# Kernel optimization log

Hardware: AMD Instinct MI355X
Metric: run time of the kernel (lower is better)

Reference implementation:

```python
import jax, jax.numpy as jnp
import numpy as np

NUM_HEADS = 8
GEM_P = 3.0
GEM_EPS = 1e-6
L2_EPS = 1e-12


def _l2norm(x):
    n = jnp.sqrt(jnp.sum(x * x, axis=-1, keepdims=True))
    return x / jnp.maximum(n, L2_EPS)


def setup_inputs() -> dict:
    key = jax.random.key(0)
    ks = jax.random.split(key, 7)
    B, Ci, H, W = 8, 256, 40, 40
    D, N = 128, 32768
    image_feat = jax.random.normal(ks[0], (B, Ci, H, W), dtype=jnp.float32)
    cloud_feat = jax.random.normal(ks[1], (N, D), dtype=jnp.float32)
    cloud_bids = jax.random.randint(ks[2], (N,), 0, B, dtype=jnp.int32)
    W1 = jax.random.normal(ks[3], (Ci, D), dtype=jnp.float32) * (1.0 / np.sqrt(Ci))
    b1 = jnp.zeros((D,), dtype=jnp.float32)
    W2 = jax.random.normal(ks[4], (D, Ci), dtype=jnp.float32) * (1.0 / np.sqrt(D))
    b2 = jnp.zeros((Ci,), dtype=jnp.float32)
    return {"image_feat": image_feat, "cloud_feat": cloud_feat, "cloud_bids": cloud_bids,
            "W1": W1, "b1": b1, "W2": W2, "b2": b2}


def _gem(x, axis):
    # generalized-mean pooling: (mean(clamp(x,eps)^p))^(1/p)
    xp = jnp.clip(x, GEM_EPS, None) ** GEM_P
    return jnp.mean(xp, axis=axis) ** (1.0 / GEM_P)


def reference(image_feat, cloud_feat, cloud_bids, W1, b1, W2, b2):
    B, Ci, H, W = image_feat.shape
    D = W1.shape[1]
    h, dh = NUM_HEADS, D // NUM_HEADS

    # image branch: permute -> linear -> tokens
    x = jnp.einsum('bchw,cd->bhwd', image_feat, W1) + b1          # [B,H,W,D]
    tok = _l2norm(x.reshape(B, H * W, D))                          # [B,HW,D]

    # window_size=1 SA: all image tokens of a batch share coord (b,0,0,0)
    # -> full self-attention per batch window; use_proj=False -> q=k=v=feats
    q = tok.reshape(B, H * W, h, dh)
    scores = jnp.einsum('bnhd,bmhd->bhnm', q, q) * (dh ** -0.5)    # [B,h,HW,HW]
    attn = jax.nn.softmax(scores, axis=-1)
    out = jnp.einsum('bhnm,bmhd->bnhd', attn, q).reshape(B, H, W, D)

    # cloud tokens: unique voxel coords -> singleton windows -> identity attention
    cloud_out = _l2norm(cloud_feat)                                # [N,D]

    # project image tokens back to image_dim channels
    img_out = jnp.einsum('bhwd,dc->bhwc', out, W2) + b2            # [B,H,W,Ci]
    img_out = jnp.transpose(img_out, (0, 3, 1, 2))                 # [B,Ci,H,W]

    # GeM pooling
    image_gem = _gem(img_out, axis=(2, 3))                         # [B,Ci]
    cp = jnp.clip(cloud_out, GEM_EPS, None) ** GEM_P
    seg = jax.ops.segment_sum(cp, cloud_bids, num_segments=B)      # [B,D]
    cnt = jax.ops.segment_sum(jnp.ones((cloud_out.shape[0], 1), cp.dtype),
                              cloud_bids, num_segments=B)
    cloud_gem = (seg / jnp.maximum(cnt, 1.0)) ** (1.0 / GEM_P)     # [B,D]

    return (img_out, cloud_out, image_gem, cloud_gem)
```

## Files before the change

### kernel.cpp

```cpp
#include <hip/hip_runtime.h>
#include <hip/hip_bf16.h>
#include <math.h>

#define BATCH 8
#define CI    256
#define HWSZ  1600
#define DDIM  128
#define NHEAD 8
#define DH    16
#define NPTS  32768

typedef __attribute__((ext_vector_type(4))) short s16x4;
typedef __attribute__((ext_vector_type(4))) float f32x4;

#if defined(__HIP_DEVICE_COMPILE__)
  #if __has_builtin(__builtin_amdgcn_mfma_f32_16x16x16bf16_1k)
    #define MFMA16(a, b, c) __builtin_amdgcn_mfma_f32_16x16x16bf16_1k(a, b, c, 0, 0, 0)
  #elif __has_builtin(__builtin_amdgcn_mfma_f32_16x16x16_bf16)
    #define MFMA16(a, b, c) __builtin_amdgcn_mfma_f32_16x16x16_bf16(a, b, c, 0, 0, 0)
  #else
    #error "no 16x16x16 bf16 mfma builtin on this device target"
  #endif
  #if __has_builtin(__builtin_amdgcn_exp2f)
    #define EXP2(x) __builtin_amdgcn_exp2f(x)
  #else
    #define EXP2(x) exp2f(x)
  #endif
#else
  #define MFMA16(a, b, c) (c)
  #define EXP2(x) (x)
#endif

union fragu {
  s16x4 s;
  unsigned int u[2];
  uint2 u2;
};

__device__ __forceinline__ unsigned int pk_bf2(float a, float b) {
  __hip_bfloat162 h = __float22bfloat162_rn(make_float2(a, b));
  return *(unsigned int*)&h;
}
__device__ __forceinline__ float bf2f(unsigned short u) {
  return __uint_as_float(((unsigned int)u) << 16);
}

__global__ __launch_bounds__(256) void kprep(
    const float* __restrict__ W1, const float* __restrict__ W2,
    const float* __restrict__ cf, const int* __restrict__ bids,
    unsigned short* __restrict__ W1s, unsigned short* __restrict__ W2s,
    float* __restrict__ cloud_out, float* __restrict__ gaw,
    float* __restrict__ cntw) {
  __shared__ float ga[BATCH * DDIM];
  __shared__ float gc[BATCH];
  int t = threadIdx.x;
  if (blockIdx.x < 64) {
    int e = blockIdx.x * 256 + t;
    int lane = e & 63, lm = lane & 15, qd = lane >> 4;
    if (e < 8192) {
      int ks = (e >> 6) & 15, dt = e >> 10;
      const float* p = W1 + (size_t)(ks * 16 + 4 * qd) * DDIM + dt * 16 + lm;
      float f0 = p[0], f1 = p[DDIM], f2 = p[2 * DDIM], f3 = p[3 * DDIM];
      *(uint2*)&W1s[(size_t)e * 4] = make_uint2(pk_bf2(f0, f1), pk_bf2(f2, f3));
    } else {
      int e2 = e - 8192;
      int ks = (e2 >> 6) & 7, ct = e2 >> 9;
      const float* p = W2 + (size_t)(ks * 16 + 4 * qd) * CI + ct * 16 + lm;
      float f0 = p[0], f1 = p[CI], f2 = p[2 * CI], f3 = p[3 * CI];
      *(uint2*)&W2s[(size_t)e2 * 4] = make_uint2(pk_bf2(f0, f1), pk_bf2(f2, f3));
    }
    return;
  }
  int bk = blockIdx.x - 64;
  for (int i = t; i < BATCH * DDIM; i += 256) ga[i] = 0.f;
  if (t < BATCH) gc[t] = 0.f;
  __syncthreads();
  for (int half = 0; half < 2; half++) {
    int r = bk * 128 + half * 64 + (t >> 2);
    int dq = (t & 3) * 32;
    const float* row = cf + (size_t)r * DDIM + dq;
    float4 v[8];
    float ss = 0.f;
#pragma unroll
    for (int j = 0; j < 8; j++) {
      v[j] = *(const float4*)(row + j * 4);
      ss += v[j].x*v[j].x + v[j].y*v[j].y + v[j].z*v[j].z + v[j].w*v[j].w;
    }
    ss += __shfl_xor(ss, 1);
    ss += __shfl_xor(ss, 2);
    float sc = 1.f / fmaxf(sqrtf(ss), 1e-12f);
    int bid = bids[r];
    if ((t & 3) == 0) atomicAdd(&gc[bid], 1.f);
    float* orow = cloud_out + (size_t)r * DDIM + dq;
    float* gb = &ga[bid * DDIM + dq];
#pragma unroll
    for (int j = 0; j < 8; j++) {
      float4 y;
      y.x = v[j].x * sc; y.y = v[j].y * sc; y.z = v[j].z * sc; y.w = v[j].w * sc;
      *(float4*)(orow + j * 4) = y;
      float c0 = fmaxf(y.x, 1e-6f), c1 = fmaxf(y.y, 1e-6f);
      float c2 = fmaxf(y.z, 1e-6f), c3 = fmaxf(y.w, 1e-6f);
      atomicAdd(&gb[j*4+0], c0*c0*c0);
      atomicAdd(&gb[j*4+1], c1*c1*c1);
      atomicAdd(&gb[j*4+2], c2*c2*c2);
      atomicAdd(&gb[j*4+3], c3*c3*c3);
    }
  }
  __syncthreads();
  for (int i = t; i < BATCH * DDIM; i += 256) gaw[(size_t)bk * 1024 + i] = ga[i];
  if (t < BATCH) cntw[bk * 8 + t] = gc[t];
}

__global__ __launch_bounds__(256) void k1_mfma(
    const float* __restrict__ img, const unsigned short* __restrict__ W1s,
    const float* __restrict__ b1, unsigned short* __restrict__ tokh) {
  int t = threadIdx.x, lane = t & 63, w = t >> 6;
  int lm = lane & 15, qd = lane >> 4;
  int blk = blockIdx.x;
  int b = blk / 25, n0 = (blk % 25) * 64;
  int tok = n0 + w * 16 + lm;
  const float* imgb = img + (size_t)b * CI * HWSZ;
  const s16x4* W1s4 = (const s16x4*)W1s;
  float fv[16][4];
#pragma unroll
  for (int ks = 0; ks < 16; ks++) {
    const float* p = imgb + (size_t)(ks * 16 + 4 * qd) * HWSZ + tok;
    fv[ks][0] = p[0];        fv[ks][1] = p[HWSZ];
    fv[ks][2] = p[2 * HWSZ]; fv[ks][3] = p[3 * HWSZ];
  }
  f32x4 acc[8];
#pragma unroll
  for (int dt = 0; dt < 8; dt++) acc[dt] = (f32x4){0.f, 0.f, 0.f, 0.f};
#pragma unroll
  for (int ks = 0; ks < 16; ks++) {
    fragu bf_;
    bf_.u[0] = pk_bf2(fv[ks][0], fv[ks][1]);
    bf_.u[1] = pk_bf2(fv[ks][2], fv[ks][3]);
#pragma unroll
    for (int dt = 0; dt < 8; dt++) {
      s16x4 af = W1s4[(dt * 16 + ks) * 64 + lane];
      acc[dt] = MFMA16(af, bf_.s, acc[dt]);
    }
  }
  float vals[8][4];
  float ss = 0.f;
#pragma unroll
  for (int dt = 0; dt < 8; dt++)
#pragma unroll
    for (int r = 0; r < 4; r++) {
      float v = acc[dt][r] + b1[dt * 16 + 4 * qd + r];
      vals[dt][r] = v;
      ss += v * v;
    }
  ss += __shfl_xor(ss, 16);
  ss += __shfl_xor(ss, 32);
  float inv = 1.f / fmaxf(sqrtf(ss), 1e-12f);
#pragma unroll
  for (int dt = 0; dt < 8; dt++) {
    uint2 pk = make_uint2(pk_bf2(vals[dt][0] * inv, vals[dt][1] * inv),
                          pk_bf2(vals[dt][2] * inv, vals[dt][3] * inv));
    *(uint2*)&tokh[(((size_t)b * NHEAD + dt) * HWSZ + tok) * DH + 4 * qd] = pk;
  }
}

#define NKC2     800
#define XK_STR   24
#define VT_STR   808
__global__ __launch_bounds__(512) void k2_attn(
    const unsigned short* __restrict__ tokh, float* __restrict__ numw,
    float* __restrict__ denw) {
  __shared__ unsigned short sXk[NKC2 * XK_STR];
  __shared__ unsigned short sVt[16 * VT_STR];
  const int gx = blockIdx.x;
  const int bh = gx >> 1, kc = gx & 1;
  const int t = threadIdx.x;
  const int lane = t & 63;
  const int w = t >> 6;
  const int lm = lane & 15;
  const int qd = lane >> 4;
  const unsigned short* tok = tokh + (size_t)bh * (HWSZ * DH);
  const int qw = blockIdx.y * 512 + w * 64;
  const bool active = qw < HWSZ;

  for (int r = t; r < NKC2; r += 512) {
    const uint4* src = (const uint4*)(tok + (size_t)(kc * NKC2 + r) * DH);
    union { uint4 u4[2]; unsigned short us[16]; } uu;
    uu.u4[0] = src[0]; uu.u4[1] = src[1];
    *(uint4*)&sXk[r * XK_STR]     = uu.u4[0];
    *(uint4*)&sXk[r * XK_STR + 8] = uu.u4[1];
#pragma unroll
    for (int d = 0; d < 16; d++) sVt[d * VT_STR + r] = uu.us[d];
  }

  const float SCL = 0.25f * 1.44269504088896f;
  s16x4 qf[4];
  f32x4 oacc[4];
  f32x4 dacc[4];
#pragma unroll
  for (int s = 0; s < 4; s++) {
    oacc[s] = (f32x4){0.f, 0.f, 0.f, 0.f};
    dacc[s] = (f32x4){0.f, 0.f, 0.f, 0.f};
  }
  if (active) {
#pragma unroll
    for (int s = 0; s < 4; s++) {
      const unsigned short* qs = tok + (size_t)(qw + s * 16 + lm) * DH + 4 * qd;
      s16x4 raw = *(const s16x4*)qs;
      fragu q;
      q.u[0] = pk_bf2(bf2f((unsigned short)raw[0]) * SCL,
                      bf2f((unsigned short)raw[1]) * SCL);
      q.u[1] = pk_bf2(bf2f((unsigned short)raw[2]) * SCL,
                      bf2f((unsigned short)raw[3]) * SCL);
      qf[s] = q.s;
    }
  }
  __syncthreads();

  if (active) {
    fragu ones;
    ones.u[0] = 0x3F803F80u;
    ones.u[1] = 0x3F803F80u;
#pragma unroll 2
    for (int st = 0; st < NKC2 / 16; st++) {
      int n0 = st * 16;
      s16x4 kf = *(const s16x4*)&sXk[(n0 + lm) * XK_STR + 4 * qd];
      s16x4 vf = *(const s16x4*)&sVt[lm * VT_STR + n0 + 4 * qd];
#pragma unroll
      for (int s = 0; s < 4; s++) {
        f32x4 sc = MFMA16(kf, qf[s], ((f32x4){0.f, 0.f, 0.f, 0.f}));
        float e0 = EXP2(sc.x), e1 = EXP2(sc.y), e2 = EXP2(sc.z), e3 = EXP2(sc.w);
        fragu pf;
        pf.u[0] = pk_bf2(e0, e1);
        pf.u[1] = pk_bf2(e2, e3);
        dacc[s] = MFMA16(ones.s, pf.s, dacc[s]);
        oacc[s] = MFMA16(vf, pf.s, oacc[s]);
      }
    }
  }

  if (active) {
#pragma unroll
    for (int s = 0; s < 4; s++) {
      size_t q = (size_t)qw + s * 16 + lm;
      float* np = numw + (((size_t)bh * 2 + kc) * HWSZ + q) * 16 + 4 * qd;
      *(f32x4*)np = oacc[s];
      if (qd == 0) denw[((size_t)bh * 2 + kc) * HWSZ + q] = dacc[s][0];
    }
  }
}

__global__ __launch_bounds__(256) void k3_mfma(
    const float* __restrict__ numw, const float* __restrict__ denw,
    const unsigned short* __restrict__ W2s, const float* __restrict__ b2,
    float* __restrict__ img_out) {
  int t = threadIdx.x, lane = t & 63, w = t >> 6;
  int lm = lane & 15, qd = lane >> 4;
  int blk = blockIdx.x;
  int b = blk / 25, n0 = (blk % 25) * 64;
  int tok = n0 + w * 16 + lm;
  const s16x4* W2s4 = (const s16x4*)W2s;
  f32x4 acc[16];
#pragma unroll
  for (int ct = 0; ct < 16; ct++) acc[ct] = (f32x4){0.f, 0.f, 0.f, 0.f};
#pragma unroll 2
  for (int ks = 0; ks < 8; ks++) {
    size_t bh2 = (size_t)(b * 8 + ks) * 2;
    const float* npb = numw + (bh2 * HWSZ + tok) * 16 + 4 * qd;
    f32x4 nv0 = *(const f32x4*)npb;
    f32x4 nv1 = *(const f32x4*)(npb + (size_t)HWSZ * 16);
    float d0 = denw[bh2 * HWSZ + tok];
    float d1 = denw[bh2 * HWSZ + HWSZ + tok];
    float inv = 1.f / (d0 + d1);
    fragu bf_;
    bf_.u[0] = pk_bf2((nv0.x + nv1.x) * inv, (nv0.y + nv1.y) * inv);
    bf_.u[1] = pk_bf2((nv0.z + nv1.z) * inv, (nv0.w + nv1.w) * inv);
#pragma unroll
    for (int ct = 0; ct < 16; ct++) {
      s16x4 af = W2s4[(ct * 8 + ks) * 64 + lane];
      acc[ct] = MFMA16(af, bf_.s, acc[ct]);
    }
  }
  float* ob = img_out + (size_t)b * CI * HWSZ;
#pragma unroll
  for (int ct = 0; ct < 16; ct++)
#pragma unroll
    for (int r = 0; r < 4; r++) {
      int ci = ct * 16 + 4 * qd + r;
      ob[(size_t)ci * HWSZ + tok] = acc[ct][r] + b2[ci];
    }
}

__global__ __launch_bounds__(256) void kpost(
    const float* __restrict__ img_out, const float* __restrict__ gaw,
    const float* __restrict__ cntw, float* __restrict__ image_gem,
    float* __restrict__ cloud_gem) {
  __shared__ float cs[BATCH];
  int t = threadIdx.x;
  if (blockIdx.x < 512) {
    int w = t >> 6, lane = t & 63;
    int row = blockIdx.x * 4 + w;
    const float* r = img_out + (size_t)row * HWSZ;
    float s = 0.f;
    for (int i = lane; i < HWSZ; i += 64) {
      float c = fmaxf(r[i], 1e-6f);
      s += c * c * c;
    }
    s += __shfl_xor(s, 1);  s += __shfl_xor(s, 2);  s += __shfl_xor(s, 4);
    s += __shfl_xor(s, 8);  s += __shfl_xor(s, 16); s += __shfl_xor(s, 32);
    if (lane == 0) image_gem[row] = powf(s * (1.f / (float)HWSZ), 1.f / 3.f);
  } else {
    int j = (blockIdx.x - 512) * 256 + t;
    if (t < BATCH) {
      float s = 0.f;
      for (int k = 0; k < 256; k++) s += cntw[k * 8 + t];
      cs[t] = s;
    }
    __syncthreads();
    float s = 0.f;
#pragma unroll 4
    for (int k = 0; k < 256; k++) s += gaw[(size_t)k * 1024 + j];
    int b = j >> 7;
    cloud_gem[j] = powf(s / fmaxf(cs[b], 1.f), 1.f / 3.f);
  }
}

extern "C" void kernel_launch(void* const* d_in, const int* in_sizes, int n_in,
                              void* d_out, int out_size, void* d_ws, size_t ws_size,
                              hipStream_t stream) {
  const float* image_feat = (const float*)d_in[0];
  const float* cloud_feat = (const float*)d_in[1];
  const int*   cloud_bids = (const int*)d_in[2];
  const float* W1 = (const float*)d_in[3];
  const float* b1 = (const float*)d_in[4];
  const float* W2 = (const float*)d_in[5];
  const float* b2 = (const float*)d_in[6];

  float* out = (float*)d_out;
  float* img_out   = out;
  float* cloud_out = out + 3276800;
  float* image_gem = out + 3276800 + 4194304;
  float* cloud_gem = image_gem + 2048;

  char* ws = (char*)d_ws;
  unsigned short* tokh = (unsigned short*)ws;
  float* numw = (float*)(ws + 3276800);
  float* denw = (float*)(ws + 16384000);
  unsigned short* W1s = (unsigned short*)(ws + 17203200);
  unsigned short* W2s = (unsigned short*)(ws + 17268736);
  float* gaw  = (float*)(ws + 17334272);
  float* cntw = (float*)(ws + 18382848);

  kprep<<<dim3(320), dim3(256), 0, stream>>>(W1, W2, cloud_feat, cloud_bids,
                                             W1s, W2s, cloud_out, gaw, cntw);
  k1_mfma<<<dim3(200), dim3(256), 0, stream>>>(image_feat, W1s, b1, tokh);
  k2_attn<<<dim3(128, 4), dim3(512), 0, stream>>>(tokh, numw, denw);
  k3_mfma<<<dim3(200), dim3(256), 0, stream>>>(numw, denw, W2s, b2, img_out);
  kpost<<<dim3(516), dim3(256), 0, stream>>>(img_out, gaw, cntw,
                                             image_gem, cloud_gem);
}
```

Baseline: 192.7 us.

## Fuse image GeM reduction into projection epilogue and move cloud work into k1

The image GeM cube-sum is now computed in the k3 epilogue from register values, using cross-lane shuffles and global atomics into a zeroed buffer. This removes kpost's second pass over the 13 MB img_out tensor. The cloud L2-norm and segment-sum blocks move from kprep into k1 as extra blocks, so they run alongside the image projection, and kprep shrinks to weight packing plus zeroing the accumulator. The cost is float atomics, which make the summation order nondeterministic, plus shuffle overhead in k3.

```diff
diff --git a/kernel.cpp b/kernel.cpp
--- a/kernel.cpp
+++ b/kernel.cpp
@@ -47,74 +47,80 @@
 
 __global__ __launch_bounds__(256) void kprep(
     const float* __restrict__ W1, const float* __restrict__ W2,
+    unsigned short* __restrict__ W1s, unsigned short* __restrict__ W2s,
+    float* __restrict__ gsum) {
+  int t = threadIdx.x;
+  if (blockIdx.x == 64) {
+    for (int i = t; i < BATCH * CI; i += 256) gsum[i] = 0.f;
+    return;
+  }
+  int e = blockIdx.x * 256 + t;
+  int lane = e & 63, lm = lane & 15, qd = lane >> 4;
+  if (e < 8192) {
+    int ks = (e >> 6) & 15, dt = e >> 10;
+    const float* p = W1 + (size_t)(ks * 16 + 4 * qd) * DDIM + dt * 16 + lm;
+    float f0 = p[0], f1 = p[DDIM], f2 = p[2 * DDIM], f3 = p[3 * DDIM];
+    *(uint2*)&W1s[(size_t)e * 4] = make_uint2(pk_bf2(f0, f1), pk_bf2(f2, f3));
+  } else {
+    int e2 = e - 8192;
+    int ks = (e2 >> 6) & 7, ct = e2 >> 9;
+    const float* p = W2 + (size_t)(ks * 16 + 4 * qd) * CI + ct * 16 + lm;
+    float f0 = p[0], f1 = p[CI], f2 = p[2 * CI], f3 = p[3 * CI];
+    *(uint2*)&W2s[(size_t)e2 * 4] = make_uint2(pk_bf2(f0, f1), pk_bf2(f2, f3));
+  }
+}
+
+__global__ __launch_bounds__(256) void k1_mfma(
+    const float* __restrict__ img, const unsigned short* __restrict__ W1s,
+    const float* __restrict__ b1, unsigned short* __restrict__ tokh,
     const float* __restrict__ cf, const int* __restrict__ bids,
-    unsigned short* __restrict__ W1s, unsigned short* __restrict__ W2s,
     float* __restrict__ cloud_out, float* __restrict__ gaw,
     float* __restrict__ cntw) {
   __shared__ float ga[BATCH * DDIM];
   __shared__ float gc[BATCH];
   int t = threadIdx.x;
-  if (blockIdx.x < 64) {
-    int e = blockIdx.x * 256 + t;
-    int lane = e & 63, lm = lane & 15, qd = lane >> 4;
-    if (e < 8192) {
-      int ks = (e >> 6) & 15, dt = e >> 10;
-      const float* p = W1 + (size_t)(ks * 16 + 4 * qd) * DDIM + dt * 16 + lm;
-      float f0 = p[0], f1 = p[DDIM], f2 = p[2 * DDIM], f3 = p[3 * DDIM];
-      *(uint2*)&W1s[(size_t)e * 4] = make_uint2(pk_bf2(f0, f1), pk_bf2(f2, f3));
-    } else {
-      int e2 = e - 8192;
-      int ks = (e2 >> 6) & 7, ct = e2 >> 9;
-      const float* p = W2 + (size_t)(ks * 16 + 4 * qd) * CI + ct * 16 + lm;
-      float f0 = p[0], f1 = p[CI], f2 = p[2 * CI], f3 = p[3 * CI];
-      *(uint2*)&W2s[(size_t)e2 * 4] = make_uint2(pk_bf2(f0, f1), pk_bf2(f2, f3));
-    }
+  if (blockIdx.x >= 200) {
+    int bk = blockIdx.x - 200;
+    for (int i = t; i < BATCH * DDIM; i += 256) ga[i] = 0.f;
+    if (t < BATCH) gc[t] = 0.f;
+    __syncthreads();
+    for (int half = 0; half < 2; half++) {
+      int r = bk * 128 + half * 64 + (t >> 2);
+      int dq = (t & 3) * 32;
+      const float* row = cf + (size_t)r * DDIM + dq;
+      float4 v[8];
+      float ss = 0.f;
+#pragma unroll
+      for (int j = 0; j < 8; j++) {
+        v[j] = *(const float4*)(row + j * 4);
+        ss += v[j].x*v[j].x + v[j].y*v[j].y + v[j].z*v[j].z + v[j].w*v[j].w;
+      }
+      ss += __shfl_xor(ss, 1);
+      ss += __shfl_xor(ss, 2);
+      float sc = 1.f / fmaxf(sqrtf(ss), 1e-12f);
+      int bid = bids[r];
+      if ((t & 3) == 0) atomicAdd(&gc[bid], 1.f);
+      float* orow = cloud_out + (size_t)r * DDIM + dq;
+      float* gb = &ga[bid * DDIM + dq];
+#pragma unroll
+      for (int j = 0; j < 8; j++) {
+        float4 y;
+        y.x = v[j].x * sc; y.y = v[j].y * sc; y.z = v[j].z * sc; y.w = v[j].w * sc;
+        *(float4*)(orow + j * 4) = y;
+        float c0 = fmaxf(y.x, 1e-6f), c1 = fmaxf(y.y, 1e-6f);
+        float c2 = fmaxf(y.z, 1e-6f), c3 = fmaxf(y.w, 1e-6f);
+        atomicAdd(&gb[j*4+0], c0*c0*c0);
+        atomicAdd(&gb[j*4+1], c1*c1*c1);
+        atomicAdd(&gb[j*4+2], c2*c2*c2);
+        atomicAdd(&gb[j*4+3], c3*c3*c3);
+      }
+    }
+    __syncthreads();
+    for (int i = t; i < BATCH * DDIM; i += 256) gaw[(size_t)bk * 1024 + i] = ga[i];
+    if (t < BATCH) cntw[bk * 8 + t] = gc[t];
     return;
   }
-  int bk = blockIdx.x - 64;
-  for (int i = t; i < BATCH * DDIM; i += 256) ga[i] = 0.f;
-  if (t < BATCH) gc[t] = 0.f;
-  __syncthreads();
-  for (int half = 0; half < 2; half++) {
-    int r = bk * 128 + half * 64 + (t >> 2);
-    int dq = (t & 3) * 32;
-    const float* row = cf + (size_t)r * DDIM + dq;
-    float4 v[8];
-    float ss = 0.f;
-#pragma unroll
-    for (int j = 0; j < 8; j++) {
-      v[j] = *(const float4*)(row + j * 4);
-      ss += v[j].x*v[j].x + v[j].y*v[j].y + v[j].z*v[j].z + v[j].w*v[j].w;
-    }
-    ss += __shfl_xor(ss, 1);
-    ss += __shfl_xor(ss, 2);
-    float sc = 1.f / fmaxf(sqrtf(ss), 1e-12f);
-    int bid = bids[r];
-    if ((t & 3) == 0) atomicAdd(&gc[bid], 1.f);
-    float* orow = cloud_out + (size_t)r * DDIM + dq;
-    float* gb = &ga[bid * DDIM + dq];
-#pragma unroll
-    for (int j = 0; j < 8; j++) {
-      float4 y;
-      y.x = v[j].x * sc; y.y = v[j].y * sc; y.z = v[j].z * sc; y.w = v[j].w * sc;
-      *(float4*)(orow + j * 4) = y;
-      float c0 = fmaxf(y.x, 1e-6f), c1 = fmaxf(y.y, 1e-6f);
-      float c2 = fmaxf(y.z, 1e-6f), c3 = fmaxf(y.w, 1e-6f);
-      atomicAdd(&gb[j*4+0], c0*c0*c0);
-      atomicAdd(&gb[j*4+1], c1*c1*c1);
-      atomicAdd(&gb[j*4+2], c2*c2*c2);
-      atomicAdd(&gb[j*4+3], c3*c3*c3);
-    }
-  }
-  __syncthreads();
-  for (int i = t; i < BATCH * DDIM; i += 256) gaw[(size_t)bk * 1024 + i] = ga[i];
-  if (t < BATCH) cntw[bk * 8 + t] = gc[t];
-}
-
-__global__ __launch_bounds__(256) void k1_mfma(
-    const float* __restrict__ img, const unsigned short* __restrict__ W1s,
-    const float* __restrict__ b1, unsigned short* __restrict__ tokh) {
-  int t = threadIdx.x, lane = t & 63, w = t >> 6;
+  int lane = t & 63, w = t >> 6;
   int lm = lane & 15, qd = lane >> 4;
   int blk = blockIdx.x;
   int b = blk / 25, n0 = (blk % 25) * 64;
@@ -252,7 +258,7 @@
 __global__ __launch_bounds__(256) void k3_mfma(
     const float* __restrict__ numw, const float* __restrict__ denw,
     const unsigned short* __restrict__ W2s, const float* __restrict__ b2,
-    float* __restrict__ img_out) {
+    float* __restrict__ img_out, float* __restrict__ gsum) {
   int t = threadIdx.x, lane = t & 63, w = t >> 6;
   int lm = lane & 15, qd = lane >> 4;
   int blk = blockIdx.x;
@@ -281,35 +287,42 @@
     }
   }
   float* ob = img_out + (size_t)b * CI * HWSZ;
-#pragma unroll
-  for (int ct = 0; ct < 16; ct++)
+  float keep[4] = {0.f, 0.f, 0.f, 0.f};
+#pragma unroll
+  for (int ct = 0; ct < 16; ct++) {
+    float vr[4];
 #pragma unroll
     for (int r = 0; r < 4; r++) {
       int ci = ct * 16 + 4 * qd + r;
-      ob[(size_t)ci * HWSZ + tok] = acc[ct][r] + b2[ci];
-    }
+      float v = acc[ct][r] + b2[ci];
+      ob[(size_t)ci * HWSZ + tok] = v;
+      float c = fmaxf(v, 1e-6f);
+      vr[r] = c * c * c;
+    }
+#pragma unroll
+    for (int r = 0; r < 4; r++) {
+      vr[r] += __shfl_xor(vr[r], 1);
+      vr[r] += __shfl_xor(vr[r], 2);
+      vr[r] += __shfl_xor(vr[r], 4);
+      vr[r] += __shfl_xor(vr[r], 8);
+    }
+    bool sel = (lm == ct);
+#pragma unroll
+    for (int r = 0; r < 4; r++) keep[r] = sel ? vr[r] : keep[r];
+  }
+#pragma unroll
+  for (int r = 0; r < 4; r++)
+    atomicAdd(&gsum[b * CI + lm * 16 + 4 * qd + r], keep[r]);
 }
 
 __global__ __launch_bounds__(256) void kpost(
-    const float* __restrict__ img_out, const float* __restrict__ gaw,
-    const float* __restrict__ cntw, float* __restrict__ image_gem,
+    const float* __restrict__ gaw, const float* __restrict__ cntw,
+    const float* __restrict__ gsum, float* __restrict__ image_gem,
     float* __restrict__ cloud_gem) {
   __shared__ float cs[BATCH];
   int t = threadIdx.x;
-  if (blockIdx.x < 512) {
-    int w = t >> 6, lane = t & 63;
-    int row = blockIdx.x * 4 + w;
-    const float* r = img_out + (size_t)row * HWSZ;
-    float s = 0.f;
-    for (int i = lane; i < HWSZ; i += 64) {
-      float c = fmaxf(r[i], 1e-6f);
-      s += c * c * c;
-    }
-    s += __shfl_xor(s, 1);  s += __shfl_xor(s, 2);  s += __shfl_xor(s, 4);
-    s += __shfl_xor(s, 8);  s += __shfl_xor(s, 16); s += __shfl_xor(s, 32);
-    if (lane == 0) image_gem[row] = powf(s * (1.f / (float)HWSZ), 1.f / 3.f);
-  } else {
-    int j = (blockIdx.x - 512) * 256 + t;
+  if (blockIdx.x < 4) {
+    int j = blockIdx.x * 256 + t;
     if (t < BATCH) {
       float s = 0.f;
       for (int k = 0; k < 256; k++) s += cntw[k * 8 + t];
@@ -321,6 +334,9 @@
     for (int k = 0; k < 256; k++) s += gaw[(size_t)k * 1024 + j];
     int b = j >> 7;
     cloud_gem[j] = powf(s / fmaxf(cs[b], 1.f), 1.f / 3.f);
+  } else {
+    for (int c = t; c < BATCH * CI; c += 256)
+      image_gem[c] = powf(gsum[c] * (1.f / (float)HWSZ), 1.f / 3.f);
   }
 }
 
@@ -349,12 +365,15 @@
   unsigned short* W2s = (unsigned short*)(ws + 17268736);
   float* gaw  = (float*)(ws + 17334272);
   float* cntw = (float*)(ws + 18382848);
-
-  kprep<<<dim3(320), dim3(256), 0, stream>>>(W1, W2, cloud_feat, cloud_bids,
-                                             W1s, W2s, cloud_out, gaw, cntw);
-  k1_mfma<<<dim3(200), dim3(256), 0, stream>>>(image_feat, W1s, b1, tokh);
+  float* gsum = (float*)(ws + 18391040);
+
+  kprep<<<dim3(65), dim3(256), 0, stream>>>(W1, W2, W1s, W2s, gsum);
+  k1_mfma<<<dim3(456), dim3(256), 0, stream>>>(image_feat, W1s, b1, tokh,
+                                               cloud_feat, cloud_bids,
+                                               cloud_out, gaw, cntw);
   k2_attn<<<dim3(128, 4), dim3(512), 0, stream>>>(tokh, numw, denw);
-  k3_mfma<<<dim3(200), dim3(256), 0, stream>>>(numw, denw, W2s, b2, img_out);
-  kpost<<<dim3(516), dim3(256), 0, stream>>>(img_out, gaw, cntw,
-                                             image_gem, cloud_gem);
-}
+  k3_mfma<<<dim3(200), dim3(256), 0, stream>>>(numw, denw, W2s, b2,
+                                               img_out, gsum);
+  kpost<<<dim3(5), dim3(256), 0, stream>>>(gaw, cntw, gsum,
+                                           image_gem, cloud_gem);
+}
```

After: 199.2 us. +3.4%, slower.

## Use full-key attention per block, normalize in-kernel, and fuse cloud branch into k1

Applied to the files above, without the earlier changes.

The attention kernel now processes all 1600 keys per block instead of splitting keys into two halves. It normalizes the output itself and writes bf16 results, so the fp32 numerator/denominator partials and their combine step in k3 go away. The cloud l2norm/GeM work moves from the prep kernel into extra blocks of k1, so it overlaps with the image projection and kprep shrinks to only the weight repacking. The trade-off is larger LDS use per attention block, half as many attention blocks, and uneven per-wave work (wave 0 handles an extra query tile).

```diff
diff --git a/kernel.cpp b/kernel.cpp
--- a/kernel.cpp
+++ b/kernel.cpp
@@ -47,74 +47,75 @@
 
 __global__ __launch_bounds__(256) void kprep(
     const float* __restrict__ W1, const float* __restrict__ W2,
+    unsigned short* __restrict__ W1s, unsigned short* __restrict__ W2s) {
+  int t = threadIdx.x;
+  int e = blockIdx.x * 256 + t;
+  int lane = e & 63, lm = lane & 15, qd = lane >> 4;
+  if (e < 8192) {
+    int ks = (e >> 6) & 15, dt = e >> 10;
+    const float* p = W1 + (size_t)(ks * 16 + 4 * qd) * DDIM + dt * 16 + lm;
+    float f0 = p[0], f1 = p[DDIM], f2 = p[2 * DDIM], f3 = p[3 * DDIM];
+    *(uint2*)&W1s[(size_t)e * 4] = make_uint2(pk_bf2(f0, f1), pk_bf2(f2, f3));
+  } else {
+    int e2 = e - 8192;
+    int ks = (e2 >> 6) & 7, ct = e2 >> 9;
+    const float* p = W2 + (size_t)(ks * 16 + 4 * qd) * CI + ct * 16 + lm;
+    float f0 = p[0], f1 = p[CI], f2 = p[2 * CI], f3 = p[3 * CI];
+    *(uint2*)&W2s[(size_t)e2 * 4] = make_uint2(pk_bf2(f0, f1), pk_bf2(f2, f3));
+  }
+}
+
+__global__ __launch_bounds__(256) void k1_mfma(
+    const float* __restrict__ img, const unsigned short* __restrict__ W1s,
+    const float* __restrict__ b1, unsigned short* __restrict__ tokh,
     const float* __restrict__ cf, const int* __restrict__ bids,
-    unsigned short* __restrict__ W1s, unsigned short* __restrict__ W2s,
     float* __restrict__ cloud_out, float* __restrict__ gaw,
     float* __restrict__ cntw) {
   __shared__ float ga[BATCH * DDIM];
   __shared__ float gc[BATCH];
   int t = threadIdx.x;
-  if (blockIdx.x < 64) {
-    int e = blockIdx.x * 256 + t;
-    int lane = e & 63, lm = lane & 15, qd = lane >> 4;
-    if (e < 8192) {
-      int ks = (e >> 6) & 15, dt = e >> 10;
-      const float* p = W1 + (size_t)(ks * 16 + 4 * qd) * DDIM + dt * 16 + lm;
-      float f0 = p[0], f1 = p[DDIM], f2 = p[2 * DDIM], f3 = p[3 * DDIM];
-      *(uint2*)&W1s[(size_t)e * 4] = make_uint2(pk_bf2(f0, f1), pk_bf2(f2, f3));
-    } else {
-      int e2 = e - 8192;
-      int ks = (e2 >> 6) & 7, ct = e2 >> 9;
-      const float* p = W2 + (size_t)(ks * 16 + 4 * qd) * CI + ct * 16 + lm;
-      float f0 = p[0], f1 = p[CI], f2 = p[2 * CI], f3 = p[3 * CI];
-      *(uint2*)&W2s[(size_t)e2 * 4] = make_uint2(pk_bf2(f0, f1), pk_bf2(f2, f3));
-    }
+  if (blockIdx.x >= 200) {
+    int bk = blockIdx.x - 200;
+    for (int i = t; i < BATCH * DDIM; i += 256) ga[i] = 0.f;
+    if (t < BATCH) gc[t] = 0.f;
+    __syncthreads();
+    for (int half = 0; half < 2; half++) {
+      int r = bk * 128 + half * 64 + (t >> 2);
+      int dq = (t & 3) * 32;
+      const float* row = cf + (size_t)r * DDIM + dq;
+      float4 v[8];
+      float ss = 0.f;
+#pragma unroll
+      for (int j = 0; j < 8; j++) {
+        v[j] = *(const float4*)(row + j * 4);
+        ss += v[j].x*v[j].x + v[j].y*v[j].y + v[j].z*v[j].z + v[j].w*v[j].w;
+      }
+      ss += __shfl_xor(ss, 1);
+      ss += __shfl_xor(ss, 2);
+      float sc = 1.f / fmaxf(sqrtf(ss), 1e-12f);
+      int bid = bids[r];
+      if ((t & 3) == 0) atomicAdd(&gc[bid], 1.f);
+      float* orow = cloud_out + (size_t)r * DDIM + dq;
+      float* gb = &ga[bid * DDIM + dq];
+#pragma unroll
+      for (int j = 0; j < 8; j++) {
+        float4 y;
+        y.x = v[j].x * sc; y.y = v[j].y * sc; y.z = v[j].z * sc; y.w = v[j].w * sc;
+        *(float4*)(orow + j * 4) = y;
+        float c0 = fmaxf(y.x, 1e-6f), c1 = fmaxf(y.y, 1e-6f);
+        float c2 = fmaxf(y.z, 1e-6f), c3 = fmaxf(y.w, 1e-6f);
+        atomicAdd(&gb[j*4+0], c0*c0*c0);
+        atomicAdd(&gb[j*4+1], c1*c1*c1);
+        atomicAdd(&gb[j*4+2], c2*c2*c2);
+        atomicAdd(&gb[j*4+3], c3*c3*c3);
+      }
+    }
+    __syncthreads();
+    for (int i = t; i < BATCH * DDIM; i += 256) gaw[(size_t)bk * 1024 + i] = ga[i];
+    if (t < BATCH) cntw[bk * 8 + t] = gc[t];
     return;
   }
-  int bk = blockIdx.x - 64;
-  for (int i = t; i < BATCH * DDIM; i += 256) ga[i] = 0.f;
-  if (t < BATCH) gc[t] = 0.f;
-  __syncthreads();
-  for (int half = 0; half < 2; half++) {
-    int r = bk * 128 + half * 64 + (t >> 2);
-    int dq = (t & 3) * 32;
-    const float* row = cf + (size_t)r * DDIM + dq;
-    float4 v[8];
-    float ss = 0.f;
-#pragma unroll
-    for (int j = 0; j < 8; j++) {
-      v[j] = *(const float4*)(row + j * 4);
-      ss += v[j].x*v[j].x + v[j].y*v[j].y + v[j].z*v[j].z + v[j].w*v[j].w;
-    }
-    ss += __shfl_xor(ss, 1);
-    ss += __shfl_xor(ss, 2);
-    float sc = 1.f / fmaxf(sqrtf(ss), 1e-12f);
-    int bid = bids[r];
-    if ((t & 3) == 0) atomicAdd(&gc[bid], 1.f);
-    float* orow = cloud_out + (size_t)r * DDIM + dq;
-    float* gb = &ga[bid * DDIM + dq];
-#pragma unroll
-    for (int j = 0; j < 8; j++) {
-      float4 y;
-      y.x = v[j].x * sc; y.y = v[j].y * sc; y.z = v[j].z * sc; y.w = v[j].w * sc;
-      *(float4*)(orow + j * 4) = y;
-      float c0 = fmaxf(y.x, 1e-6f), c1 = fmaxf(y.y, 1e-6f);
-      float c2 = fmaxf(y.z, 1e-6f), c3 = fmaxf(y.w, 1e-6f);
-      atomicAdd(&gb[j*4+0], c0*c0*c0);
-      atomicAdd(&gb[j*4+1], c1*c1*c1);
-      atomicAdd(&gb[j*4+2], c2*c2*c2);
-      atomicAdd(&gb[j*4+3], c3*c3*c3);
-    }
-  }
-  __syncthreads();
-  for (int i = t; i < BATCH * DDIM; i += 256) gaw[(size_t)bk * 1024 + i] = ga[i];
-  if (t < BATCH) cntw[bk * 8 + t] = gc[t];
-}
-
-__global__ __launch_bounds__(256) void k1_mfma(
-    const float* __restrict__ img, const unsigned short* __restrict__ W1s,
-    const float* __restrict__ b1, unsigned short* __restrict__ tokh) {
-  int t = threadIdx.x, lane = t & 63, w = t >> 6;
+  int lane = t & 63, w = t >> 6;
   int lm = lane & 15, qd = lane >> 4;
   int blk = blockIdx.x;
   int b = blk / 25, n0 = (blk % 25) * 64;
@@ -163,27 +164,24 @@
   }
 }
 
-#define NKC2     800
-#define XK_STR   24
-#define VT_STR   808
+#define NKT     1600
+#define XK_STR  24
+#define VT_STR  1608
 __global__ __launch_bounds__(512) void k2_attn(
-    const unsigned short* __restrict__ tokh, float* __restrict__ numw,
-    float* __restrict__ denw) {
-  __shared__ unsigned short sXk[NKC2 * XK_STR];
+    const unsigned short* __restrict__ tokh, unsigned short* __restrict__ aout) {
+  __shared__ unsigned short sXk[NKT * XK_STR];
   __shared__ unsigned short sVt[16 * VT_STR];
-  const int gx = blockIdx.x;
-  const int bh = gx >> 1, kc = gx & 1;
+  const int bh = blockIdx.x;
+  const int strip = blockIdx.y;
   const int t = threadIdx.x;
   const int lane = t & 63;
   const int w = t >> 6;
   const int lm = lane & 15;
   const int qd = lane >> 4;
   const unsigned short* tok = tokh + (size_t)bh * (HWSZ * DH);
-  const int qw = blockIdx.y * 512 + w * 64;
-  const bool active = qw < HWSZ;
-
-  for (int r = t; r < NKC2; r += 512) {
-    const uint4* src = (const uint4*)(tok + (size_t)(kc * NKC2 + r) * DH);
+
+  for (int r = t; r < NKT; r += 512) {
+    const uint4* src = (const uint4*)(tok + (size_t)r * DH);
     union { uint4 u4[2]; unsigned short us[16]; } uu;
     uu.u4[0] = src[0]; uu.u4[1] = src[1];
     *(uint4*)&sXk[r * XK_STR]     = uu.u4[0];
@@ -194,63 +192,70 @@
 
   const float SCL = 0.25f * 1.44269504088896f;
   s16x4 qf[4];
-  f32x4 oacc[4];
-  f32x4 dacc[4];
+  f32x4 oacc[4], dacc[4];
 #pragma unroll
   for (int s = 0; s < 4; s++) {
     oacc[s] = (f32x4){0.f, 0.f, 0.f, 0.f};
     dacc[s] = (f32x4){0.f, 0.f, 0.f, 0.f};
-  }
-  if (active) {
-#pragma unroll
-    for (int s = 0; s < 4; s++) {
-      const unsigned short* qs = tok + (size_t)(qw + s * 16 + lm) * DH + 4 * qd;
+    int ti = w + 8 * s;
+    if (ti < 25) {
+      int q = strip * 400 + ti * 16 + lm;
+      const unsigned short* qs = tok + (size_t)q * DH + 4 * qd;
       s16x4 raw = *(const s16x4*)qs;
-      fragu q;
-      q.u[0] = pk_bf2(bf2f((unsigned short)raw[0]) * SCL,
-                      bf2f((unsigned short)raw[1]) * SCL);
-      q.u[1] = pk_bf2(bf2f((unsigned short)raw[2]) * SCL,
-                      bf2f((unsigned short)raw[3]) * SCL);
-      qf[s] = q.s;
+      fragu qq;
+      qq.u[0] = pk_bf2(bf2f((unsigned short)raw[0]) * SCL,
+                       bf2f((unsigned short)raw[1]) * SCL);
+      qq.u[1] = pk_bf2(bf2f((unsigned short)raw[2]) * SCL,
+                       bf2f((unsigned short)raw[3]) * SCL);
+      qf[s] = qq.s;
     }
   }
   __syncthreads();
 
-  if (active) {
-    fragu ones;
-    ones.u[0] = 0x3F803F80u;
-    ones.u[1] = 0x3F803F80u;
+  fragu ones;
+  ones.u[0] = 0x3F803F80u;
+  ones.u[1] = 0x3F803F80u;
 #pragma unroll 2
-    for (int st = 0; st < NKC2 / 16; st++) {
-      int n0 = st * 16;
-      s16x4 kf = *(const s16x4*)&sXk[(n0 + lm) * XK_STR + 4 * qd];
-      s16x4 vf = *(const s16x4*)&sVt[lm * VT_STR + n0 + 4 * qd];
-#pragma unroll
-      for (int s = 0; s < 4; s++) {
-        f32x4 sc = MFMA16(kf, qf[s], ((f32x4){0.f, 0.f, 0.f, 0.f}));
-        float e0 = EXP2(sc.x), e1 = EXP2(sc.y), e2 = EXP2(sc.z), e3 = EXP2(sc.w);
-        fragu pf;
-        pf.u[0] = pk_bf2(e0, e1);
-        pf.u[1] = pk_bf2(e2, e3);
-        dacc[s] = MFMA16(ones.s, pf.s, dacc[s]);
-        oacc[s] = MFMA16(vf, pf.s, oacc[s]);
-      }
-    }
-  }
-
-  if (active) {
-#pragma unroll
-    for (int s = 0; s < 4; s++) {
-      size_t q = (size_t)qw + s * 16 + lm;
-      float* np = numw + (((size_t)bh * 2 + kc) * HWSZ + q) * 16 + 4 * qd;
-      *(f32x4*)np = oacc[s];
-      if (qd == 0) denw[((size_t)bh * 2 + kc) * HWSZ + q] = dacc[s][0];
+  for (int st = 0; st < NKT / 16; st++) {
+    int n0 = st * 16;
+    s16x4 kf = *(const s16x4*)&sXk[(n0 + lm) * XK_STR + 4 * qd];
+    s16x4 vf = *(const s16x4*)&sVt[lm * VT_STR + n0 + 4 * qd];
+#pragma unroll
+    for (int s = 0; s < 3; s++) {
+      f32x4 sc = MFMA16(kf, qf[s], ((f32x4){0.f, 0.f, 0.f, 0.f}));
+      float e0 = EXP2(sc.x), e1 = EXP2(sc.y), e2 = EXP2(sc.z), e3 = EXP2(sc.w);
+      fragu pf;
+      pf.u[0] = pk_bf2(e0, e1);
+      pf.u[1] = pk_bf2(e2, e3);
+      dacc[s] = MFMA16(ones.s, pf.s, dacc[s]);
+      oacc[s] = MFMA16(vf, pf.s, oacc[s]);
+    }
+    if (w == 0) {
+      f32x4 sc = MFMA16(kf, qf[3], ((f32x4){0.f, 0.f, 0.f, 0.f}));
+      float e0 = EXP2(sc.x), e1 = EXP2(sc.y), e2 = EXP2(sc.z), e3 = EXP2(sc.w);
+      fragu pf;
+      pf.u[0] = pk_bf2(e0, e1);
+      pf.u[1] = pk_bf2(e2, e3);
+      dacc[3] = MFMA16(ones.s, pf.s, dacc[3]);
+      oacc[3] = MFMA16(vf, pf.s, oacc[3]);
+    }
+  }
+
+#pragma unroll
+  for (int s = 0; s < 4; s++) {
+    int ti = w + 8 * s;
+    if (ti < 25) {
+      int q = strip * 400 + ti * 16 + lm;
+      float inv = 1.f / dacc[s][0];
+      uint2 pk = make_uint2(pk_bf2(oacc[s][0] * inv, oacc[s][1] * inv),
+                            pk_bf2(oacc[s][2] * inv, oacc[s][3] * inv));
+      *(uint2*)&aout[((size_t)bh * HWSZ + q) * DH + 4 * qd] = pk;
     }
   }
 }
 
 __global__ __launch_bounds__(256) void k3_mfma(
-    const float* __restrict__ numw, const float* __restrict__ denw,
+    const unsigned short* __restrict__ aout,
     const unsigned short* __restrict__ W2s, const float* __restrict__ b2,
     float* __restrict__ img_out) {
   int t = threadIdx.x, lane = t & 63, w = t >> 6;
@@ -262,22 +267,13 @@
   f32x4 acc[16];
 #pragma unroll
   for (int ct = 0; ct < 16; ct++) acc[ct] = (f32x4){0.f, 0.f, 0.f, 0.f};
-#pragma unroll 2
+#pragma unroll
   for (int ks = 0; ks < 8; ks++) {
-    size_t bh2 = (size_t)(b * 8 + ks) * 2;
-    const float* npb = numw + (bh2 * HWSZ + tok) * 16 + 4 * qd;
-    f32x4 nv0 = *(const f32x4*)npb;
-    f32x4 nv1 = *(const f32x4*)(npb + (size_t)HWSZ * 16);
-    float d0 = denw[bh2 * HWSZ + tok];
-    float d1 = denw[bh2 * HWSZ + HWSZ + tok];
-    float inv = 1.f / (d0 + d1);
-    fragu bf_;
-    bf_.u[0] = pk_bf2((nv0.x + nv1.x) * inv, (nv0.y + nv1.y) * inv);
-    bf_.u[1] = pk_bf2((nv0.z + nv1.z) * inv, (nv0.w + nv1.w) * inv);
+    s16x4 bf_ = *(const s16x4*)&aout[(((size_t)(b * NHEAD + ks)) * HWSZ + tok) * DH + 4 * qd];
 #pragma unroll
     for (int ct = 0; ct < 16; ct++) {
       s16x4 af = W2s4[(ct * 8 + ks) * 64 + lane];
-      acc[ct] = MFMA16(af, bf_.s, acc[ct]);
+      acc[ct] = MFMA16(af, bf_, acc[ct]);
     }
   }
   float* ob = img_out + (size_t)b * CI * HWSZ;
@@ -343,18 +339,18 @@
 
   char* ws = (char*)d_ws;
   unsigned short* tokh = (unsigned short*)ws;
-  float* numw = (float*)(ws + 3276800);
-  float* denw = (float*)(ws + 16384000);
-  unsigned short* W1s = (unsigned short*)(ws + 17203200);
-  unsigned short* W2s = (unsigned short*)(ws + 17268736);
-  float* gaw  = (float*)(ws + 17334272);
-  float* cntw = (float*)(ws + 18382848);
-
-  kprep<<<dim3(320), dim3(256), 0, stream>>>(W1, W2, cloud_feat, cloud_bids,
-                                             W1s, W2s, cloud_out, gaw, cntw);
-  k1_mfma<<<dim3(200), dim3(256), 0, stream>>>(image_feat, W1s, b1, tokh);
-  k2_attn<<<dim3(128, 4), dim3(512), 0, stream>>>(tokh, numw, denw);
-  k3_mfma<<<dim3(200), dim3(256), 0, stream>>>(numw, denw, W2s, b2, img_out);
+  unsigned short* aout = (unsigned short*)(ws + 3276800);
+  unsigned short* W1s  = (unsigned short*)(ws + 6553600);
+  unsigned short* W2s  = (unsigned short*)(ws + 6619136);
+  float* gaw  = (float*)(ws + 6684672);
+  float* cntw = (float*)(ws + 7733248);
+
+  kprep<<<dim3(64), dim3(256), 0, stream>>>(W1, W2, W1s, W2s);
+  k1_mfma<<<dim3(456), dim3(256), 0, stream>>>(image_feat, W1s, b1, tokh,
+                                               cloud_feat, cloud_bids,
+                                               cloud_out, gaw, cntw);
+  k2_attn<<<dim3(64, 4), dim3(512), 0, stream>>>(tokh, aout);
+  k3_mfma<<<dim3(200), dim3(256), 0, stream>>>(aout, W2s, b2, img_out);
   kpost<<<dim3(516), dim3(256), 0, stream>>>(img_out, gaw, cntw,
                                              image_gem, cloud_gem);
 }
```

New measurement: 207.4 us. +7.6%, slower.

## Split attention keys four ways and tile queries into full 400-token strips

Applied to the files above, without the earlier changes.

The attention kernel now splits each head's keys into four chunks of 400 instead of two chunks of 800. Queries are tiled as 400-token strips of 25 16-row tiles spread over 8 waves. The one leftover tile per strip rotates across waves by chunk and strip. This removes the waves that sat idle in the last query strip and doubles the grid, for better occupancy and load balance. In exchange the numerator and denominator partials double in size, so the projection kernel reads and sums four partials, and the workspace layout is shifted.

```diff
diff --git a/kernel.cpp b/kernel.cpp
--- a/kernel.cpp
+++ b/kernel.cpp
@@ -163,27 +163,27 @@
   }
 }
 
-#define NKC2     800
+#define NKC4     400
 #define XK_STR   24
-#define VT_STR   808
+#define VT_STR   408
 __global__ __launch_bounds__(512) void k2_attn(
     const unsigned short* __restrict__ tokh, float* __restrict__ numw,
     float* __restrict__ denw) {
-  __shared__ unsigned short sXk[NKC2 * XK_STR];
+  __shared__ unsigned short sXk[NKC4 * XK_STR];
   __shared__ unsigned short sVt[16 * VT_STR];
   const int gx = blockIdx.x;
-  const int bh = gx >> 1, kc = gx & 1;
+  const int bh = gx >> 2, kc = gx & 3;
+  const int strip = blockIdx.y;
   const int t = threadIdx.x;
   const int lane = t & 63;
   const int w = t >> 6;
   const int lm = lane & 15;
   const int qd = lane >> 4;
+  const int wx = (kc + strip * 4) & 7;
   const unsigned short* tok = tokh + (size_t)bh * (HWSZ * DH);
-  const int qw = blockIdx.y * 512 + w * 64;
-  const bool active = qw < HWSZ;
-
-  for (int r = t; r < NKC2; r += 512) {
-    const uint4* src = (const uint4*)(tok + (size_t)(kc * NKC2 + r) * DH);
+
+  for (int r = t; r < NKC4; r += 512) {
+    const uint4* src = (const uint4*)(tok + (size_t)(kc * NKC4 + r) * DH);
     union { uint4 u4[2]; unsigned short us[16]; } uu;
     uu.u4[0] = src[0]; uu.u4[1] = src[1];
     *(uint4*)&sXk[r * XK_STR]     = uu.u4[0];
@@ -194,57 +194,63 @@
 
   const float SCL = 0.25f * 1.44269504088896f;
   s16x4 qf[4];
-  f32x4 oacc[4];
-  f32x4 dacc[4];
+  f32x4 oacc[4], dacc[4];
 #pragma unroll
   for (int s = 0; s < 4; s++) {
     oacc[s] = (f32x4){0.f, 0.f, 0.f, 0.f};
     dacc[s] = (f32x4){0.f, 0.f, 0.f, 0.f};
-  }
-  if (active) {
-#pragma unroll
-    for (int s = 0; s < 4; s++) {
-      const unsigned short* qs = tok + (size_t)(qw + s * 16 + lm) * DH + 4 * qd;
+    int ti = (s < 3) ? (w + 8 * s) : 24;
+    if (s < 3 || w == wx) {
+      int q = strip * 400 + ti * 16 + lm;
+      const unsigned short* qs = tok + (size_t)q * DH + 4 * qd;
       s16x4 raw = *(const s16x4*)qs;
-      fragu q;
-      q.u[0] = pk_bf2(bf2f((unsigned short)raw[0]) * SCL,
-                      bf2f((unsigned short)raw[1]) * SCL);
-      q.u[1] = pk_bf2(bf2f((unsigned short)raw[2]) * SCL,
-                      bf2f((unsigned short)raw[3]) * SCL);
-      qf[s] = q.s;
+      fragu qq;
+      qq.u[0] = pk_bf2(bf2f((unsigned short)raw[0]) * SCL,
+                       bf2f((unsigned short)raw[1]) * SCL);
+      qq.u[1] = pk_bf2(bf2f((unsigned short)raw[2]) * SCL,
+                       bf2f((unsigned short)raw[3]) * SCL);
+      qf[s] = qq.s;
     }
   }
   __syncthreads();
 
-  if (active) {
-    fragu ones;
-    ones.u[0] = 0x3F803F80u;
-    ones.u[1] = 0x3F803F80u;
+  fragu ones;
+  ones.u[0] = 0x3F803F80u;
+  ones.u[1] = 0x3F803F80u;
 #pragma unroll 2
-    for (int st = 0; st < NKC2 / 16; st++) {
-      int n0 = st * 16;
-      s16x4 kf = *(const s16x4*)&sXk[(n0 + lm) * XK_STR + 4 * qd];
-      s16x4 vf = *(const s16x4*)&sVt[lm * VT_STR + n0 + 4 * qd];
-#pragma unroll
-      for (int s = 0; s < 4; s++) {
-        f32x4 sc = MFMA16(kf, qf[s], ((f32x4){0.f, 0.f, 0.f, 0.f}));
-        float e0 = EXP2(sc.x), e1 = EXP2(sc.y), e2 = EXP2(sc.z), e3 = EXP2(sc.w);
-        fragu pf;
-        pf.u[0] = pk_bf2(e0, e1);
-        pf.u[1] = pk_bf2(e2, e3);
-        dacc[s] = MFMA16(ones.s, pf.s, dacc[s]);
-        oacc[s] = MFMA16(vf, pf.s, oacc[s]);
-      }
-    }
-  }
-
-  if (active) {
-#pragma unroll
-    for (int s = 0; s < 4; s++) {
-      size_t q = (size_t)qw + s * 16 + lm;
-      float* np = numw + (((size_t)bh * 2 + kc) * HWSZ + q) * 16 + 4 * qd;
+  for (int st = 0; st < NKC4 / 16; st++) {
+    int n0 = st * 16;
+    s16x4 kf = *(const s16x4*)&sXk[(n0 + lm) * XK_STR + 4 * qd];
+    s16x4 vf = *(const s16x4*)&sVt[lm * VT_STR + n0 + 4 * qd];
+#pragma unroll
+    for (int s = 0; s < 3; s++) {
+      f32x4 sc = MFMA16(kf, qf[s], ((f32x4){0.f, 0.f, 0.f, 0.f}));
+      float e0 = EXP2(sc.x), e1 = EXP2(sc.y), e2 = EXP2(sc.z), e3 = EXP2(sc.w);
+      fragu pf;
+      pf.u[0] = pk_bf2(e0, e1);
+      pf.u[1] = pk_bf2(e2, e3);
+      dacc[s] = MFMA16(ones.s, pf.s, dacc[s]);
+      oacc[s] = MFMA16(vf, pf.s, oacc[s]);
+    }
+    if (w == wx) {
+      f32x4 sc = MFMA16(kf, qf[3], ((f32x4){0.f, 0.f, 0.f, 0.f}));
+      float e0 = EXP2(sc.x), e1 = EXP2(sc.y), e2 = EXP2(sc.z), e3 = EXP2(sc.w);
+      fragu pf;
+      pf.u[0] = pk_bf2(e0, e1);
+      pf.u[1] = pk_bf2(e2, e3);
+      dacc[3] = MFMA16(ones.s, pf.s, dacc[3]);
+      oacc[3] = MFMA16(vf, pf.s, oacc[3]);
+    }
+  }
+
+#pragma unroll
+  for (int s = 0; s < 4; s++) {
+    int ti = (s < 3) ? (w + 8 * s) : 24;
+    if (s < 3 || w == wx) {
+      size_t q = (size_t)strip * 400 + ti * 16 + lm;
+      float* np = numw + (((size_t)bh * 4 + kc) * HWSZ + q) * 16 + 4 * qd;
       *(f32x4*)np = oacc[s];
-      if (qd == 0) denw[((size_t)bh * 2 + kc) * HWSZ + q] = dacc[s][0];
+      if (qd == 0) denw[((size_t)bh * 4 + kc) * HWSZ + q] = dacc[s][0];
     }
   }
 }
@@ -264,16 +270,23 @@
   for (int ct = 0; ct < 16; ct++) acc[ct] = (f32x4){0.f, 0.f, 0.f, 0.f};
 #pragma unroll 2
   for (int ks = 0; ks < 8; ks++) {
-    size_t bh2 = (size_t)(b * 8 + ks) * 2;
-    const float* npb = numw + (bh2 * HWSZ + tok) * 16 + 4 * qd;
+    size_t bh4 = (size_t)(b * 8 + ks) * 4;
+    const float* npb = numw + (bh4 * HWSZ + tok) * 16 + 4 * qd;
+    const float* dpb = denw + bh4 * HWSZ + tok;
     f32x4 nv0 = *(const f32x4*)npb;
     f32x4 nv1 = *(const f32x4*)(npb + (size_t)HWSZ * 16);
-    float d0 = denw[bh2 * HWSZ + tok];
-    float d1 = denw[bh2 * HWSZ + HWSZ + tok];
-    float inv = 1.f / (d0 + d1);
+    f32x4 nv2 = *(const f32x4*)(npb + (size_t)HWSZ * 32);
+    f32x4 nv3 = *(const f32x4*)(npb + (size_t)HWSZ * 48);
+    float d = dpb[0] + dpb[HWSZ] + dpb[2 * HWSZ] + dpb[3 * HWSZ];
+    float inv = 1.f / d;
+    f32x4 nv;
+    nv.x = (nv0.x + nv1.x) + (nv2.x + nv3.x);
+    nv.y = (nv0.y + nv1.y) + (nv2.y + nv3.y);
+    nv.z = (nv0.z + nv1.z) + (nv2.z + nv3.z);
+    nv.w = (nv0.w + nv1.w) + (nv2.w + nv3.w);
     fragu bf_;
-    bf_.u[0] = pk_bf2((nv0.x + nv1.x) * inv, (nv0.y + nv1.y) * inv);
-    bf_.u[1] = pk_bf2((nv0.z + nv1.z) * inv, (nv0.w + nv1.w) * inv);
+    bf_.u[0] = pk_bf2(nv.x * inv, nv.y * inv);
+    bf_.u[1] = pk_bf2(nv.z * inv, nv.w * inv);
 #pragma unroll
     for (int ct = 0; ct < 16; ct++) {
       s16x4 af = W2s4[(ct * 8 + ks) * 64 + lane];
@@ -344,16 +357,16 @@
   char* ws = (char*)d_ws;
   unsigned short* tokh = (unsigned short*)ws;
   float* numw = (float*)(ws + 3276800);
-  float* denw = (float*)(ws + 16384000);
-  unsigned short* W1s = (unsigned short*)(ws + 17203200);
-  unsigned short* W2s = (unsigned short*)(ws + 17268736);
-  float* gaw  = (float*)(ws + 17334272);
-  float* cntw = (float*)(ws + 18382848);
+  float* denw = (float*)(ws + 29491200);
+  unsigned short* W1s = (unsigned short*)(ws + 31129600);
+  unsigned short* W2s = (unsigned short*)(ws + 31195136);
+  float* gaw  = (float*)(ws + 31260672);
+  float* cntw = (float*)(ws + 32309248);
 
   kprep<<<dim3(320), dim3(256), 0, stream>>>(W1, W2, cloud_feat, cloud_bids,
                                              W1s, W2s, cloud_out, gaw, cntw);
   k1_mfma<<<dim3(200), dim3(256), 0, stream>>>(image_feat, W1s, b1, tokh);
-  k2_attn<<<dim3(128, 4), dim3(512), 0, stream>>>(tokh, numw, denw);
+  k2_attn<<<dim3(256, 4), dim3(512), 0, stream>>>(tokh, numw, denw);
   k3_mfma<<<dim3(200), dim3(256), 0, stream>>>(numw, denw, W2s, b2, img_out);
   kpost<<<dim3(516), dim3(256), 0, stream>>>(img_out, gaw, cntw,
                                              image_gem, cloud_gem);
```

New measurement: 188.1 us. 1.02x faster.
